# Kernel tuning notes

Measured on AMD Instinct MI355X. Metric: run time of the kernel, lower is better.

## Reference

```python
import jax, jax.numpy as jnp
import numpy as np

V = 50257  # vocab_size
H = 512    # d_model
S = 512    # source length
B = 8      # batch
T = 64     # decode steps


def setup_inputs() -> dict:
    key = jax.random.key(0)
    k1, k2, k3, k4, k5, k6 = jax.random.split(key, 6)
    src_full = jax.random.randint(k1, (S, B), 0, V, dtype=jnp.int32)
    decode_output = jax.random.normal(k2, (T, B, H), dtype=jnp.float32)
    decode_attn = jax.random.uniform(k3, (B, T, S), dtype=jnp.float32)
    memory = jax.random.normal(k4, (S, B, H), dtype=jnp.float32)
    # learned params: gen_proj (H->V) and prob_proj (H->1)
    W_gen = jax.random.normal(k5, (H, V), dtype=jnp.float32) / np.sqrt(H)
    b_gen = jnp.zeros((V,), dtype=jnp.float32)
    W_prob = jax.random.normal(k6, (H, 1), dtype=jnp.float32) / np.sqrt(H)
    b_prob = jnp.zeros((1,), dtype=jnp.float32)
    return {
        "src_full": src_full,
        "decode_output": decode_output,
        "decode_attn": decode_attn,
        "memory": memory,
        "W_gen": W_gen,
        "b_gen": b_gen,
        "W_prob": W_prob,
        "b_prob": b_prob,
    }


def reference(src_full, decode_output, decode_attn, memory, W_gen, b_gen, W_prob, b_prob):
    # context[t,b,h] = sum_s attn[b,t,s] * memory[s,b,h]
    context = jnp.einsum("bts,sbh->tbh", decode_attn, memory)  # [T,B,H]
    prob = jax.nn.sigmoid(context @ W_prob + b_prob)           # [T,B,1] copy gate p_gen
    gen_logits = prob * jax.nn.softmax(decode_output @ W_gen + b_gen, axis=-1)  # [T,B,V]

    # scatter-add attention mass onto vocab slots: copy[t,b, src_full[s,b]] += attn[b,t,s]
    attn_tbs = jnp.transpose(decode_attn, (1, 0, 2))  # [T,B,S]
    idx = src_full.T                                  # [B,S]
    ti = jnp.arange(T)[:, None, None]
    bi = jnp.arange(B)[None, :, None]
    copy_logits = jnp.zeros((T, B, V), dtype=decode_attn.dtype).at[ti, bi, idx[None, :, :]].add(attn_tbs)
    copy_logits = (1.0 - prob) * jax.nn.softmax(copy_logits, axis=-1)

    return jnp.log(gen_logits + copy_logits)
```

## Files before the change

kernel.cpp:

```cpp
#include <hip/hip_runtime.h>
#include <hip/hip_bf16.h>
#include <math.h>

#define VV 50257
#define VP 50304
#define HH 512
#define SS 512
#define BB 8
#define TT 64
#define MM (TT*BB)

typedef __bf16 bf16x2 __attribute__((ext_vector_type(2)));
typedef __bf16 bf16x4 __attribute__((ext_vector_type(4)));
typedef __bf16 bf16x8 __attribute__((ext_vector_type(8)));
typedef float  f32x4  __attribute__((ext_vector_type(4)));

__device__ __forceinline__ __bf16 f2b(float f) {
    unsigned u = __builtin_bit_cast(unsigned, f);
    unsigned r = (u + 0x7fffu + ((u >> 16) & 1u)) >> 16;
    unsigned short s = (unsigned short)r;
    return __builtin_bit_cast(__bf16, s);
}

__device__ __forceinline__ void gl2lds16(const void* g, void* l) {
    __builtin_amdgcn_global_load_lds(
        (const __attribute__((address_space(1))) unsigned*)g,
        (__attribute__((address_space(3))) unsigned*)l, 16, 0, 0);
}

__global__ __launch_bounds__(256) void k_castA(const float* __restrict__ A,
                                               __bf16* __restrict__ Ab) {
    int i = (blockIdx.x * 256 + threadIdx.x) * 4;
    float4 v = *(const float4*)&A[i];
    bf16x4 o = {f2b(v.x), f2b(v.y), f2b(v.z), f2b(v.w)};
    *(bf16x4*)&Ab[i] = o;
}

__global__ __launch_bounds__(256) void k_castWT(const float* __restrict__ W,
                                                __bf16* __restrict__ Wt) {
    __shared__ float tile[64][65];
    int n0 = blockIdx.x * 64;
    int k0 = blockIdx.y * 64;
    int tid = threadIdx.x;
#pragma unroll
    for (int i = 0; i < 16; i++) {
        int idx = tid + i * 256;
        int kk = idx >> 6, nn = idx & 63;
        int n = n0 + nn;
        tile[kk][nn] = (n < VV) ? W[(size_t)(k0 + kk) * VV + n] : 0.f;
    }
    __syncthreads();
#pragma unroll
    for (int i = 0; i < 8; i++) {
        int idx = tid + i * 256;
        int nn = idx >> 5, kp = idx & 31;
        bf16x2 o = {f2b(tile[2 * kp][nn]), f2b(tile[2 * kp + 1][nn])};
        *(bf16x2*)&Wt[(size_t)(n0 + nn) * HH + k0 + 2 * kp] = o;
    }
}

__global__ void k_mw(const float* __restrict__ mem, const float* __restrict__ Wp,
                     float* __restrict__ mw) {
    int row = blockIdx.x;
    int lane = threadIdx.x;
    const float* mp = mem + (size_t)row * HH;
    float acc = 0.f;
#pragma unroll
    for (int i = 0; i < HH / 64; i++)
        acc += mp[lane + 64 * i] * Wp[lane + 64 * i];
#pragma unroll
    for (int off = 32; off > 0; off >>= 1) acc += __shfl_down(acc, off);
    if (lane == 0) mw[row] = acc;
}

__global__ void k_prob(const float* __restrict__ attn, const float* __restrict__ mw,
                       const float* __restrict__ bp, float* __restrict__ prob) {
    int r = blockIdx.x;
    int t = r / BB, b = r % BB;
    int lane = threadIdx.x;
    const float* ap = attn + ((size_t)b * TT + t) * SS;
    float acc = 0.f;
#pragma unroll
    for (int i = 0; i < SS / 64; i++) {
        int s = lane + 64 * i;
        acc += ap[s] * mw[s * BB + b];
    }
#pragma unroll
    for (int off = 32; off > 0; off >>= 1) acc += __shfl_down(acc, off);
    if (lane == 0) prob[r] = 1.f / (1.f + expf(-(acc + bp[0])));
}

template<bool BF16OUT>
__global__ __launch_bounds__(256, 2) void k_gemm3(const __bf16* __restrict__ Ab,
                                                  const __bf16* __restrict__ Wt,
                                                  const float* __restrict__ bias,
                                                  float* __restrict__ Cf,
                                                  __bf16* __restrict__ Cb,
                                                  float* __restrict__ Zrow) {
    __shared__ __bf16 As[2][8192];
    __shared__ __bf16 Bs[2][8192];
    __shared__ float zred[128];

    const int tid  = threadIdx.x;
    const int lane = tid & 63;
    const int wave = tid >> 6;
    const int l15  = lane & 15;
    const int quad = lane >> 4;
    const int wr = (wave >> 1) * 64;
    const int wc = (wave & 1) * 64;
    const int row0 = blockIdx.x * 128;
    const int col0 = blockIdx.y * 128;

    size_t offA[2][2], offB[2][2];
#pragma unroll
    for (int q = 0; q < 2; q++)
#pragma unroll
        for (int j = 0; j < 2; j++) {
            int seg = 2 * wave + q;
            offA[q][j] = (size_t)(row0 + seg * 16 + l15) * HH + (j * 4 + quad) * 8;
            offB[q][j] = (size_t)(col0 + seg * 16 + l15) * HH + (j * 4 + quad) * 8;
        }

#define STAGE(buf, k0)                                                        \
    do {                                                                      \
        _Pragma("unroll") for (int q = 0; q < 2; q++)                         \
        _Pragma("unroll") for (int j = 0; j < 2; j++) {                       \
            int seg = 2 * wave + q;                                           \
            gl2lds16(Ab + offA[q][j] + (k0), &As[buf][seg * 1024 + j * 512]); \
            gl2lds16(Wt + offB[q][j] + (k0), &Bs[buf][seg * 1024 + j * 512]); \
        }                                                                     \
    } while (0)

    f32x4 acc[4][4] = {};

    STAGE(0, 0);
    for (int it = 0; it < 8; ++it) {
        __syncthreads();
        if (it != 7) STAGE((it + 1) & 1, (it + 1) * 64);
        const __bf16* Al = &As[it & 1][0];
        const __bf16* Bl = &Bs[it & 1][0];
#pragma unroll
        for (int h = 0; h < 2; ++h) {
            bf16x8 af[4], bfv[4];
#pragma unroll
            for (int mt = 0; mt < 4; mt++)
                af[mt] = *(const bf16x8*)&Al[((wr >> 4) + mt) * 1024 + h * 512 + lane * 8];
#pragma unroll
            for (int nt = 0; nt < 4; nt++)
                bfv[nt] = *(const bf16x8*)&Bl[((wc >> 4) + nt) * 1024 + h * 512 + lane * 8];
#pragma unroll
            for (int mt = 0; mt < 4; mt++)
#pragma unroll
                for (int nt = 0; nt < 4; nt++)
                    acc[mt][nt] = __builtin_amdgcn_mfma_f32_16x16x32_bf16(
                        af[mt], bfv[nt], acc[mt][nt], 0, 0, 0);
        }
    }
#undef STAGE

    __syncthreads();
    if (tid < 128) zred[tid] = 0.f;
    __syncthreads();

#pragma unroll
    for (int mt = 0; mt < 4; mt++) {
        float esum[4] = {0.f, 0.f, 0.f, 0.f};
#pragma unroll
        for (int nt = 0; nt < 4; nt++) {
            int c = col0 + wc + nt * 16 + l15;
            if (c < VV) {
                float bv = bias[c];
#pragma unroll
                for (int i = 0; i < 4; i++) {
                    int r = row0 + wr + mt * 16 + quad * 4 + i;
                    float l = acc[mt][nt][i] + bv;
                    if (BF16OUT) Cb[(size_t)r * VP + c] = f2b(l);
                    else         Cf[(size_t)r * VV + c] = l;
                    esum[i] += __expf(l);
                }
            }
        }
#pragma unroll
        for (int i = 0; i < 4; i++) {
            float e = esum[i];
            e += __shfl_xor(e, 1);
            e += __shfl_xor(e, 2);
            e += __shfl_xor(e, 4);
            e += __shfl_xor(e, 8);
            if (l15 == 0)
                atomicAdd(&zred[wr + mt * 16 + quad * 4 + i], e);
        }
    }
    __syncthreads();
    if (tid < 128) atomicAdd(&Zrow[row0 + tid], zred[tid]);
}

#define HT 1024
#define NBW 1572

__device__ __forceinline__ void build_hash(const int* __restrict__ src,
                                           const float* __restrict__ ap,
                                           int b, int tid,
                                           int* keys, float* vals, unsigned* bmap,
                                           float* red, int* s_D, float* s_Zc) {
    for (int i = tid; i < HT; i += 256) { keys[i] = -1; vals[i] = 0.f; }
    for (int i = tid; i < NBW; i += 256) bmap[i] = 0u;
    if (tid == 0) *s_D = 0;
    __syncthreads();

    for (int s = tid; s < SS; s += 256) {
        int idx = src[s * BB + b];
        float v = ap[s];
        unsigned h = ((unsigned)idx * 2654435761u) >> 22;
        while (true) {
            int old = atomicCAS(&keys[h], -1, idx);
            if (old == -1 || old == idx) { atomicAdd(&vals[h], v); break; }
            h = (h + 1) & (HT - 1);
        }
    }
    __syncthreads();

    float lsum = 0.f; int dloc = 0;
    for (int i = tid; i < HT; i += 256) {
        int k = keys[i];
        if (k != -1) {
            lsum += __expf(vals[i]); dloc++;
            atomicOr(&bmap[(unsigned)k >> 5], 1u << (k & 31));
        }
    }
    atomicAdd(s_D, dloc);
    red[tid] = lsum; __syncthreads();
    for (int st = 128; st > 0; st >>= 1) {
        if (tid < st) red[tid] += red[tid + st];
        __syncthreads();
    }
    if (tid == 0) *s_Zc = (float)(VV - *s_D) + red[0];
    __syncthreads();
}

#define CHUNKV 6288
__global__ __launch_bounds__(256) void k_final_v(const int* __restrict__ src,
                                                 const float* __restrict__ attn,
                                                 const float* __restrict__ prob,
                                                 const float* __restrict__ Zrow,
                                                 const __bf16* __restrict__ LG,
                                                 float* __restrict__ out) {
    __shared__ int      keys[HT];
    __shared__ float    vals[HT];
    __shared__ unsigned bmap[NBW];
    __shared__ float    red[256];
    __shared__ int      s_D;
    __shared__ float    s_Zc;

    int r = blockIdx.y;
    int t = r / BB, b = r % BB;
    int tid = threadIdx.x;
    const float* ap = attn + ((size_t)b * TT + t) * SS;
    build_hash(src, ap, b, tid, keys, vals, bmap, red, &s_D, &s_Zc);

    float p = prob[r];
    float pinvZ = p / Zrow[r];
    float qinvZc = (1.f - p) / s_Zc;

    int c0 = blockIdx.x * CHUNKV;
    const __bf16* lrow = LG + (size_t)r * VP + c0;
    float* orow = out + (size_t)r * VV;

    for (int v0 = tid * 8; v0 < CHUNKV; v0 += 2048) {
        bf16x8 l8 = *(const bf16x8*)&lrow[v0];
#pragma unroll
        for (int e = 0; e < 8; e++) {
            int v = c0 + v0 + e;
            if (v < VV) {
                float l = (float)l8[e];
                float c = 1.f;
                if ((bmap[v >> 5] >> (v & 31)) & 1u) {
                    unsigned h = ((unsigned)v * 2654435761u) >> 22;
                    while (true) {
                        int k = keys[h];
                        if (k == v) { c = __expf(vals[h]); break; }
                        if (k == -1) break;
                        h = (h + 1) & (HT - 1);
                    }
                }
                orow[v] = __logf(pinvZ * __expf(l) + qinvZc * c);
            }
        }
    }
}

#define CHUNKS 6283
__global__ __launch_bounds__(256) void k_final_s(const int* __restrict__ src,
                                                 const float* __restrict__ attn,
                                                 const float* __restrict__ prob,
                                                 const float* __restrict__ Zrow,
                                                 float* __restrict__ out) {
    __shared__ int      keys[HT];
    __shared__ float    vals[HT];
    __shared__ unsigned bmap[NBW];
    __shared__ float    red[256];
    __shared__ int      s_D;
    __shared__ float    s_Zc;

    int r = blockIdx.y;
    int t = r / BB, b = r % BB;
    int tid = threadIdx.x;
    const float* ap = attn + ((size_t)b * TT + t) * SS;
    build_hash(src, ap, b, tid, keys, vals, bmap, red, &s_D, &s_Zc);

    float p = prob[r];
    float pinvZ = p / Zrow[r];
    float qinvZc = (1.f - p) / s_Zc;

    int c0 = blockIdx.x * CHUNKS;
    int c1 = c0 + CHUNKS; if (c1 > VV) c1 = VV;
    float* rowp = out + (size_t)r * VV;

    for (int v = c0 + tid; v < c1; v += 256) {
        float l = rowp[v];
        float c = 1.f;
        if ((bmap[v >> 5] >> (v & 31)) & 1u) {
            unsigned h = ((unsigned)v * 2654435761u) >> 22;
            while (true) {
                int k = keys[h];
                if (k == v) { c = __expf(vals[h]); break; }
                if (k == -1) break;
                h = (h + 1) & (HT - 1);
            }
        }
        rowp[v] = __logf(pinvZ * __expf(l) + qinvZc * c);
    }
}

extern "C" void kernel_launch(void* const* d_in, const int* in_sizes, int n_in,
                              void* d_out, int out_size, void* d_ws, size_t ws_size,
                              hipStream_t stream) {
    const int*   src_full      = (const int*)d_in[0];
    const float* decode_output = (const float*)d_in[1];
    const float* decode_attn   = (const float*)d_in[2];
    const float* memory        = (const float*)d_in[3];
    const float* W_gen         = (const float*)d_in[4];
    const float* b_gen         = (const float*)d_in[5];
    const float* W_prob        = (const float*)d_in[6];
    const float* b_prob        = (const float*)d_in[7];
    float* out = (float*)d_out;

    float* ws   = (float*)d_ws;
    float* mw   = ws;
    float* prob = ws + 4096;
    float* Z    = ws + 4608;
    __bf16* Ab  = (__bf16*)(ws + 5120);
    __bf16* Wt  = (__bf16*)(ws + 5120 + 131072);
    __bf16* LG  = Wt + (size_t)VP * HH;

    size_t base_b = (size_t)(5120 + 131072) * sizeof(float);
    size_t wt_b   = (size_t)VP * HH * 2;
    size_t lg_b   = (size_t)MM * VP * 2;
    bool full = ws_size >= base_b + wt_b + lg_b;

    k_castA<<<MM * HH / (256 * 4), 256, 0, stream>>>(decode_output, Ab);
    k_mw<<<SS * BB, 64, 0, stream>>>(memory, W_prob, mw);
    k_prob<<<TT * BB, 64, 0, stream>>>(decode_attn, mw, b_prob, prob);
    hipMemsetAsync(Z, 0, MM * sizeof(float), stream);

    dim3 tgrid(VP / 64, HH / 64);
    k_castWT<<<tgrid, 256, 0, stream>>>(W_gen, Wt);

    dim3 ggrid(MM / 128, VP / 128);
    if (full) {
        k_gemm3<true><<<ggrid, 256, 0, stream>>>(Ab, Wt, b_gen, nullptr, LG, Z);
        dim3 fgrid(VP / CHUNKV, MM);
        k_final_v<<<fgrid, 256, 0, stream>>>(src_full, decode_attn, prob, Z, LG, out);
    } else {
        k_gemm3<false><<<ggrid, 256, 0, stream>>>(Ab, Wt, b_gen, out, nullptr, Z);
        dim3 fgrid((VV + CHUNKS - 1) / CHUNKS, MM);
        k_final_s<<<fgrid, 256, 0, stream>>>(src_full, decode_attn, prob, Z, out);
    }
}
```

Baseline: 380.3 us.

## Widen GEMM to 8 waves with XCD-aware tile remap, one block per row in final

The GEMM block grows to 512 threads (8 waves, each computing a 64x32 sub-tile), and block IDs are remapped so that consecutive tiles sharing W columns land on the same XCD, which should improve L2 reuse. The final kernel now uses one 1024-thread block per output row instead of eight chunk blocks per row, so the scatter hash is built only once per row rather than once per chunk. The tradeoff is fewer resident blocks for the final pass, a fixed grid size assumed by the remap math, and changed register pressure in the GEMM.

```diff
diff --git a/kernel.cpp b/kernel.cpp
--- a/kernel.cpp
+++ b/kernel.cpp
@@ -91,7 +91,7 @@
 }
 
 template<bool BF16OUT>
-__global__ __launch_bounds__(256, 2) void k_gemm3(const __bf16* __restrict__ Ab,
+__global__ __launch_bounds__(512, 4) void k_gemm3(const __bf16* __restrict__ Ab,
                                                   const __bf16* __restrict__ Wt,
                                                   const float* __restrict__ bias,
                                                   float* __restrict__ Cf,
@@ -106,32 +106,31 @@
     const int wave = tid >> 6;
     const int l15  = lane & 15;
     const int quad = lane >> 4;
-    const int wr = (wave >> 1) * 64;
-    const int wc = (wave & 1) * 64;
-    const int row0 = blockIdx.x * 128;
-    const int col0 = blockIdx.y * 128;
-
-    size_t offA[2][2], offB[2][2];
-#pragma unroll
-    for (int q = 0; q < 2; q++)
-#pragma unroll
-        for (int j = 0; j < 2; j++) {
-            int seg = 2 * wave + q;
-            offA[q][j] = (size_t)(row0 + seg * 16 + l15) * HH + (j * 4 + quad) * 8;
-            offB[q][j] = (size_t)(col0 + seg * 16 + l15) * HH + (j * 4 + quad) * 8;
-        }
-
-#define STAGE(buf, k0)                                                        \
-    do {                                                                      \
-        _Pragma("unroll") for (int q = 0; q < 2; q++)                         \
-        _Pragma("unroll") for (int j = 0; j < 2; j++) {                       \
-            int seg = 2 * wave + q;                                           \
-            gl2lds16(Ab + offA[q][j] + (k0), &As[buf][seg * 1024 + j * 512]); \
-            gl2lds16(Wt + offB[q][j] + (k0), &Bs[buf][seg * 1024 + j * 512]); \
-        }                                                                     \
+    const int wr = (wave >> 2) * 64;
+    const int wc = (wave & 3) * 32;
+
+    int L = blockIdx.x + gridDim.x * blockIdx.y;
+    int xcd = L & 7, i8 = L >> 3;
+    int nid = (xcd < 4 ? xcd * 197 : 4 * 197 + (xcd - 4) * 196) + i8;
+    const int row0 = (nid & 3) * 128;
+    const int col0 = (nid >> 2) * 128;
+
+    size_t offA[2], offB[2];
+#pragma unroll
+    for (int j = 0; j < 2; j++) {
+        offA[j] = (size_t)(row0 + wave * 16 + l15) * HH + (j * 4 + quad) * 8;
+        offB[j] = (size_t)(col0 + wave * 16 + l15) * HH + (j * 4 + quad) * 8;
+    }
+
+#define STAGE(buf, k0)                                                    \
+    do {                                                                  \
+        _Pragma("unroll") for (int j = 0; j < 2; j++) {                   \
+            gl2lds16(Ab + offA[j] + (k0), &As[buf][wave * 1024 + j * 512]); \
+            gl2lds16(Wt + offB[j] + (k0), &Bs[buf][wave * 1024 + j * 512]); \
+        }                                                                 \
     } while (0)
 
-    f32x4 acc[4][4] = {};
+    f32x4 acc[4][2] = {};
 
     STAGE(0, 0);
     for (int it = 0; it < 8; ++it) {
@@ -141,17 +140,17 @@
         const __bf16* Bl = &Bs[it & 1][0];
 #pragma unroll
         for (int h = 0; h < 2; ++h) {
-            bf16x8 af[4], bfv[4];
+            bf16x8 af[4], bfv[2];
 #pragma unroll
             for (int mt = 0; mt < 4; mt++)
                 af[mt] = *(const bf16x8*)&Al[((wr >> 4) + mt) * 1024 + h * 512 + lane * 8];
 #pragma unroll
-            for (int nt = 0; nt < 4; nt++)
+            for (int nt = 0; nt < 2; nt++)
                 bfv[nt] = *(const bf16x8*)&Bl[((wc >> 4) + nt) * 1024 + h * 512 + lane * 8];
 #pragma unroll
             for (int mt = 0; mt < 4; mt++)
 #pragma unroll
-                for (int nt = 0; nt < 4; nt++)
+                for (int nt = 0; nt < 2; nt++)
                     acc[mt][nt] = __builtin_amdgcn_mfma_f32_16x16x32_bf16(
                         af[mt], bfv[nt], acc[mt][nt], 0, 0, 0);
         }
@@ -166,7 +165,7 @@
     for (int mt = 0; mt < 4; mt++) {
         float esum[4] = {0.f, 0.f, 0.f, 0.f};
 #pragma unroll
-        for (int nt = 0; nt < 4; nt++) {
+        for (int nt = 0; nt < 2; nt++) {
             int c = col0 + wc + nt * 16 + l15;
             if (c < VV) {
                 float bv = bias[c];
@@ -238,39 +237,72 @@
     __syncthreads();
 }
 
-#define CHUNKV 6288
-__global__ __launch_bounds__(256) void k_final_v(const int* __restrict__ src,
-                                                 const float* __restrict__ attn,
-                                                 const float* __restrict__ prob,
-                                                 const float* __restrict__ Zrow,
-                                                 const __bf16* __restrict__ LG,
-                                                 float* __restrict__ out) {
+__global__ __launch_bounds__(1024) void k_final_row(const int* __restrict__ src,
+                                                    const float* __restrict__ attn,
+                                                    const float* __restrict__ prob,
+                                                    const float* __restrict__ Zrow,
+                                                    const __bf16* __restrict__ LG,
+                                                    float* __restrict__ out) {
     __shared__ int      keys[HT];
     __shared__ float    vals[HT];
     __shared__ unsigned bmap[NBW];
-    __shared__ float    red[256];
+    __shared__ float    red[1024];
     __shared__ int      s_D;
     __shared__ float    s_Zc;
 
-    int r = blockIdx.y;
+    int r = blockIdx.x;
     int t = r / BB, b = r % BB;
     int tid = threadIdx.x;
     const float* ap = attn + ((size_t)b * TT + t) * SS;
-    build_hash(src, ap, b, tid, keys, vals, bmap, red, &s_D, &s_Zc);
+
+    { int i = tid; keys[i] = -1; vals[i] = 0.f; }
+    for (int i = tid; i < NBW; i += 1024) bmap[i] = 0u;
+    if (tid == 0) s_D = 0;
+    __syncthreads();
+
+    if (tid < SS) {
+        int idx = src[tid * BB + b];
+        float v = ap[tid];
+        unsigned h = ((unsigned)idx * 2654435761u) >> 22;
+        while (true) {
+            int old = atomicCAS(&keys[h], -1, idx);
+            if (old == -1 || old == idx) { atomicAdd(&vals[h], v); break; }
+            h = (h + 1) & (HT - 1);
+        }
+    }
+    __syncthreads();
+
+    float lsum = 0.f;
+    {
+        int k = keys[tid];
+        bool occ = (k != -1);
+        if (occ) {
+            lsum = __expf(vals[tid]);
+            atomicOr(&bmap[(unsigned)k >> 5], 1u << (k & 31));
+        }
+        unsigned long long m = __ballot(occ);
+        if ((tid & 63) == 0) atomicAdd(&s_D, __popcll(m));
+    }
+    red[tid] = lsum; __syncthreads();
+    for (int st = 512; st > 0; st >>= 1) {
+        if (tid < st) red[tid] += red[tid + st];
+        __syncthreads();
+    }
+    if (tid == 0) s_Zc = (float)(VV - s_D) + red[0];
+    __syncthreads();
 
     float p = prob[r];
     float pinvZ = p / Zrow[r];
     float qinvZc = (1.f - p) / s_Zc;
 
-    int c0 = blockIdx.x * CHUNKV;
-    const __bf16* lrow = LG + (size_t)r * VP + c0;
+    const __bf16* lrow = LG + (size_t)r * VP;
     float* orow = out + (size_t)r * VV;
 
-    for (int v0 = tid * 8; v0 < CHUNKV; v0 += 2048) {
+    for (int v0 = tid * 8; v0 < VP; v0 += 8192) {
         bf16x8 l8 = *(const bf16x8*)&lrow[v0];
 #pragma unroll
         for (int e = 0; e < 8; e++) {
-            int v = c0 + v0 + e;
+            int v = v0 + e;
             if (v < VV) {
                 float l = (float)l8[e];
                 float c = 1.f;
@@ -368,11 +400,10 @@
 
     dim3 ggrid(MM / 128, VP / 128);
     if (full) {
-        k_gemm3<true><<<ggrid, 256, 0, stream>>>(Ab, Wt, b_gen, nullptr, LG, Z);
-        dim3 fgrid(VP / CHUNKV, MM);
-        k_final_v<<<fgrid, 256, 0, stream>>>(src_full, decode_attn, prob, Z, LG, out);
+        k_gemm3<true><<<ggrid, 512, 0, stream>>>(Ab, Wt, b_gen, nullptr, LG, Z);
+        k_final_row<<<MM, 1024, 0, stream>>>(src_full, decode_attn, prob, Z, LG, out);
     } else {
-        k_gemm3<false><<<ggrid, 256, 0, stream>>>(Ab, Wt, b_gen, out, nullptr, Z);
+        k_gemm3<false><<<ggrid, 512, 0, stream>>>(Ab, Wt, b_gen, out, nullptr, Z);
         dim3 fgrid((VV + CHUNKS - 1) / CHUNKS, MM);
         k_final_s<<<fgrid, 256, 0, stream>>>(src_full, decode_attn, prob, Z, out);
     }
```

Result: faster. 364.8 us (-4.1%).
